# Performance work log

Measured on AMD Instinct MI355X. Metric: run time of the kernel, lower is better.

## Reference

```python
import jax, jax.numpy as jnp
import numpy as np

H = 1024
V = 32000
L = 15
B = 512


def setup_inputs() -> dict:
    key = jax.random.key(0)
    ks = jax.random.split(key, 16)
    s = 0.02
    return {
        "input_ids": jax.random.randint(ks[0], (B,), 0, V),
        "hidden": jax.random.normal(ks[1], (1, B, H), jnp.float32),
        "encoder_outputs": jax.random.normal(ks[2], (L, B, H), jnp.float32),
        "max_length": L,
        "embedding": jax.random.normal(ks[3], (V, H), jnp.float32) * s,
        "attn1_w": jax.random.normal(ks[4], (1, 2 * H), jnp.float32) * s,
        "attn1_b": jnp.zeros((1,), jnp.float32),
        "combine_w": jax.random.normal(ks[5], (H, 2 * H), jnp.float32) * s,
        "combine_b": jnp.zeros((H,), jnp.float32),
        "w_ih": jax.random.normal(ks[6], (3 * H, H), jnp.float32) * s,
        "w_hh": jax.random.normal(ks[7], (3 * H, H), jnp.float32) * s,
        "b_ih": jnp.zeros((3 * H,), jnp.float32),
        "b_hh": jnp.zeros((3 * H,), jnp.float32),
        "out_w": jax.random.normal(ks[8], (V, H), jnp.float32) * s,
        "out_b": jnp.zeros((V,), jnp.float32),
    }


def reference(input_ids, hidden, encoder_outputs, max_length, embedding,
              attn1_w, attn1_b, combine_w, combine_b,
              w_ih, w_hh, b_ih, b_hh, out_w, out_b):
    # embedding lookup (dropout is identity in eval mode)
    emb = embedding[input_ids]                       # [B, H]
    # Bahdanau-style additive scores: vectorize the per-step python loop
    emb_l = jnp.broadcast_to(emb[None], (max_length, B, H))   # [L, B, H]
    cat = jnp.concatenate([emb_l, encoder_outputs], axis=-1)  # [L, B, 2H]
    scores = cat @ attn1_w.T + attn1_b               # [L, B, 1]
    attn_weights = jax.nn.softmax(scores, axis=0)    # softmax over L
    ctx = jnp.sum(attn_weights * encoder_outputs, axis=0)     # [B, H]
    x = jnp.concatenate([emb, ctx], axis=-1) @ combine_w.T + combine_b  # [B, H]
    # n_layers = 1: relu then one GRU step (seq len 1)
    x = jax.nn.relu(x)
    h = hidden[0]                                    # [B, H]
    gi = x @ w_ih.T + b_ih                           # [B, 3H]
    gh = h @ w_hh.T + b_hh                           # [B, 3H]
    i_r, i_z, i_n = jnp.split(gi, 3, axis=1)
    h_r, h_z, h_n = jnp.split(gh, 3, axis=1)
    r = jax.nn.sigmoid(i_r + h_r)
    z = jax.nn.sigmoid(i_z + h_z)
    n = jnp.tanh(i_n + r * h_n)
    h_new = (1.0 - z) * n + z * h                    # [B, H]
    logits = h_new @ out_w.T + out_b                 # [B, V]
    output = jax.nn.log_softmax(logits, axis=1)
    return output, h_new[None], attn_weights
```

## Files before the change

### kernel.cpp

```cpp
#include <hip/hip_runtime.h>

#define HH 1024
#define VV 32000
#define LL 15
#define BB 512

typedef __bf16 bf16;
typedef __bf16 bf16x4 __attribute__((ext_vector_type(4)));
typedef __bf16 bf16x8 __attribute__((ext_vector_type(8)));
typedef float f32x4 __attribute__((ext_vector_type(4)));

#define VMCNT(n) asm volatile("s_waitcnt vmcnt(" #n ")" ::: "memory")
#define SBAR     __builtin_amdgcn_s_barrier()
#define SCHED0   __builtin_amdgcn_sched_barrier(0)

__device__ __forceinline__ unsigned short f2bf(float f) {
    unsigned int u = __float_as_uint(f);
    unsigned int r = (u + 0x7fffu + ((u >> 16) & 1u)) >> 16;
    return (unsigned short)r;
}

__device__ __forceinline__ void gld_lds16(const void* g, void* l) {
    __builtin_amdgcn_global_load_lds(
        (const __attribute__((address_space(1))) unsigned int*)g,
        (__attribute__((address_space(3))) unsigned int*)l, 16, 0, 0);
}

__global__ __launch_bounds__(256)
void pack_w(const float* __restrict__ src, unsigned short* __restrict__ dst) {
    const int bid = blockIdx.x;
    const int g = bid >> 3, rq = bid & 7;
    const float* s0 = src + ((size_t)g * 128 + rq * 16) * 1024;
    unsigned short* d0 = dst + (size_t)g * (16 * 128 * 64);
    #pragma unroll
    for (int j = 0; j < 16; j++) {
        const int s4 = j * 256 + threadIdx.x;
        const f32x4 v = ((const f32x4*)s0)[s4];
        const int sp = s4 * 4;
        const int rl = rq * 16 + (sp >> 10);
        const int k = sp & 1023;
        bf16x4 w = __builtin_convertvector(v, bf16x4);
        *(bf16x4*)&d0[(size_t)(k >> 6) * 8192 + rl * 64 + (k & 63)] = w;
    }
}

__global__ __launch_bounds__(256)
void cvt4_kernel(const float* __restrict__ a0, unsigned short* __restrict__ o0, int n0_,
                 const float* __restrict__ a1, unsigned short* __restrict__ o1, int n1_,
                 const float* __restrict__ a2, unsigned short* __restrict__ o2, int n2_,
                 const float* __restrict__ a3, unsigned short* __restrict__ o3, int n3_) {
    int i = blockIdx.x * 256 + threadIdx.x;
    const float* src; unsigned short* dst;
    if (i < n0_) { src = a0; dst = o0; }
    else if ((i -= n0_) < n1_) { src = a1; dst = o1; }
    else if ((i -= n1_) < n2_) { src = a2; dst = o2; }
    else if ((i -= n2_) < n3_) { src = a3; dst = o3; }
    else return;
    const f32x4 a = ((const f32x4*)src)[2 * i], b = ((const f32x4*)src)[2 * i + 1];
    ((bf16x4*)dst)[2 * i]     = __builtin_convertvector(a, bf16x4);
    ((bf16x4*)dst)[2 * i + 1] = __builtin_convertvector(b, bf16x4);
}

__global__ __launch_bounds__(256)
void attn_kernel(const int* __restrict__ ids, const float* __restrict__ enc,
                 const float* __restrict__ embedding,
                 const float* __restrict__ attn1_w, const float* __restrict__ attn1_b,
                 float* __restrict__ attn_out, unsigned short* __restrict__ cat_out) {
    const int b = blockIdx.x, tid = threadIdx.x;
    const int lane = tid & 63, wv = tid >> 6;

    __shared__ float s_enc[LL * HH];
    __shared__ float s_scores[LL];
    __shared__ float s_red[4];

    for (int idx = tid; idx < LL * HH / 4; idx += 256) {
        const int l = (idx * 4) >> 10, h = (idx * 4) & (HH - 1);
        *(f32x4*)&s_enc[idx * 4] = *(const f32x4*)&enc[((size_t)l * BB + b) * HH + h];
    }

    const float* embr = embedding + (size_t)ids[b] * HH;
    float p = 0.f;
    for (int j = tid; j < HH; j += 256) p += embr[j] * attn1_w[j];
    #pragma unroll
    for (int o = 32; o; o >>= 1) p += __shfl_xor(p, o);
    if (lane == 0) s_red[wv] = p;
    __syncthreads();
    const float semb = s_red[0] + s_red[1] + s_red[2] + s_red[3] + attn1_b[0];

    for (int l = wv; l < LL; l += 4) {
        float q = 0.f;
        for (int j = lane; j < HH; j += 64) q += s_enc[l * HH + j] * attn1_w[HH + j];
        #pragma unroll
        for (int o = 32; o; o >>= 1) q += __shfl_xor(q, o);
        if (lane == 0) s_scores[l] = q + semb;
    }
    __syncthreads();

    float mx = -3.4e38f;
    #pragma unroll
    for (int l = 0; l < LL; l++) mx = fmaxf(mx, s_scores[l]);
    float aw[LL], sum = 0.f;
    #pragma unroll
    for (int l = 0; l < LL; l++) { aw[l] = __expf(s_scores[l] - mx); sum += aw[l]; }
    const float inv = 1.f / sum;
    #pragma unroll
    for (int l = 0; l < LL; l++) aw[l] *= inv;

    if (tid < LL) attn_out[tid * BB + b] = aw[tid];

    for (int j = tid; j < HH; j += 256) {
        float c = 0.f;
        #pragma unroll
        for (int l = 0; l < LL; l++) c += aw[l] * s_enc[l * HH + j];
        cat_out[(size_t)b * (2 * HH) + j] = f2bf(embr[j]);
        cat_out[(size_t)b * (2 * HH) + HH + j] = f2bf(c);
    }
}

template<int TM, int TN, int OUT, int GATES>
__global__ __launch_bounds__(256)
void gemm_nt(const bf16* __restrict__ A, const bf16* __restrict__ B,
             const float* __restrict__ bias, void* __restrict__ Cout,
             const bf16* __restrict__ A2, const bf16* __restrict__ B2,
             const float* __restrict__ bias2, void* __restrict__ C2,
             const int K, const int N) {
    constexpr int FM = TM / 32, FN = TN / 32;
    __shared__ bf16 As[2][TM * 64];
    __shared__ bf16 Bs[2][TN * 64];

    if (GATES && blockIdx.z == 1) { A = A2; B = B2; bias = bias2; Cout = C2; }

    const int tid = threadIdx.x;
    const int lane = tid & 63, wave = tid >> 6;
    const int wm = wave >> 1, wn = wave & 1;
    const int rlo = lane & 15, khi = lane >> 4;
    const int m0 = blockIdx.y * TM, n0 = blockIdx.x * TN;

    f32x4 acc[FM][FN] = {};
    constexpr int IA = TM / 32, IB = TN / 32;

    auto stage = [&](int k0, int buf) {
        #pragma unroll
        for (int i = 0; i < IA; i++) {
            const int p = (i * 256 + tid) * 16;
            const int row = p >> 7;
            const int qs = (p & 127) ^ ((row & 7) << 4);
            gld_lds16(A + (size_t)(m0 + row) * K + k0 + (qs >> 1),
                      &As[buf][0] + i * 2048 + wave * 512);
        }
        #pragma unroll
        for (int i = 0; i < IB; i++) {
            const int p = (i * 256 + tid) * 16;
            const int row = p >> 7;
            const int qs = (p & 127) ^ ((row & 7) << 4);
            gld_lds16(B + (size_t)(n0 + row) * K + k0 + (qs >> 1),
                      &Bs[buf][0] + i * 2048 + wave * 512);
        }
    };

    auto compute = [&](int buf) {
        #pragma unroll
        for (int ks = 0; ks < 2; ks++) {
            bf16x8 af[FM], bfr[FN];
            #pragma unroll
            for (int m = 0; m < FM; m++) {
                const int r = wm * (TM / 2) + m * 16 + rlo;
                const int sw = (ks * 64 + khi * 16) ^ ((r & 7) << 4);
                af[m] = *(const bf16x8*)((const char*)&As[buf][0] + r * 128 + sw);
            }
            #pragma unroll
            for (int n = 0; n < FN; n++) {
                const int r = wn * (TN / 2) + n * 16 + rlo;
                const int sw = (ks * 64 + khi * 16) ^ ((r & 7) << 4);
                bfr[n] = *(const bf16x8*)((const char*)&Bs[buf][0] + r * 128 + sw);
            }
            #pragma unroll
            for (int m = 0; m < FM; m++)
                #pragma unroll
                for (int n = 0; n < FN; n++)
                    acc[m][n] = __builtin_amdgcn_mfma_f32_16x16x32_bf16(af[m], bfr[n], acc[m][n], 0, 0, 0);
        }
    };

    const int NT = K >> 6;
    stage(0, 0);
    stage(64, 1);

    for (int kt = 0; kt < NT; kt += 2) {
        {
            const int t = kt;
            if (t + 1 < NT) { VMCNT(4); } else { VMCNT(0); }
            SCHED0; SBAR; SCHED0;
            compute(0);
            SCHED0; SBAR; SCHED0;
            if (t + 2 < NT) stage((t + 2) << 6, 0);
        }
        {
            const int t = kt + 1;
            if (t + 1 < NT) { VMCNT(4); } else { VMCNT(0); }
            SCHED0; SBAR; SCHED0;
            compute(1);
            SCHED0; SBAR; SCHED0;
            if (t + 2 < NT) stage((t + 2) << 6, 1);
        }
    }

    #pragma unroll
    for (int m = 0; m < FM; m++) {
        const int gr = m0 + wm * (TM / 2) + m * 16 + khi * 4;
        #pragma unroll
        for (int n = 0; n < FN; n++) {
            const int gc = n0 + wn * (TN / 2) + n * 16 + rlo;
            const float bv = bias[gc];
            #pragma unroll
            for (int j = 0; j < 4; j++) {
                float v = acc[m][n][j] + bv;
                if (OUT == 1) {
                    v = fmaxf(v, 0.f);
                    ((unsigned short*)Cout)[(size_t)(gr + j) * N + gc] = f2bf(v);
                } else {
                    ((float*)Cout)[(size_t)(gr + j) * N + gc] = v;
                }
            }
        }
    }
}

__global__ __launch_bounds__(256, 2)
void gemm_out(const bf16* __restrict__ A, const bf16* __restrict__ Bp,
              const float* __restrict__ bias, float* __restrict__ C,
              float* __restrict__ pmax, float* __restrict__ psum) {
    constexpr int K = HH, N = VV;
    __shared__ bf16 As[2][128 * 64];
    __shared__ bf16 Bs[2][128 * 64];
    __shared__ float sPm[2][128], sPs[2][128];

    const int tid = threadIdx.x;
    const int lane = tid & 63, wave = tid >> 6;
    const int wm = wave >> 1, wn = wave & 1;
    const int rlo = lane & 15, khi = lane >> 4;

    constexpr int gridN = 250;
    constexpr int nFull = (gridN >> 3) << 5;
    const int bidx = blockIdx.x;
    int g, jm;
    if (bidx < nFull) { const int s = bidx >> 5, rem = bidx & 31; jm = rem >> 3; g = s * 8 + (rem & 7); }
    else { const int rem = bidx - nFull; constexpr int gleft = gridN & 7; g = (gridN & ~7) + rem % gleft; jm = rem / gleft; }
    const int n0 = g * 128, m0 = jm * 128;

    const char* pb = (const char*)(Bp + (size_t)g * 131072);

    f32x4 acc[4][4] = {};

    auto stage = [&](int k0, int buf) {
        #pragma unroll
        for (int i = 0; i < 4; i++) {
            const int p = (i * 256 + tid) * 16;
            const int row = p >> 7;
            const int qs = (p & 127) ^ ((row & 7) << 4);
            gld_lds16(A + (size_t)(m0 + row) * K + k0 + (qs >> 1),
                      &As[buf][0] + i * 2048 + wave * 512);
        }
        #pragma unroll
        for (int i = 0; i < 4; i++) {
            const int p = (i * 256 + tid) * 16;
            const int row = p >> 7;
            const int qs = (p & 127) ^ ((row & 7) << 4);
            gld_lds16(pb + (size_t)(k0 >> 6) * 16384 + row * 128 + qs,
                      &Bs[buf][0] + i * 2048 + wave * 512);
        }
    };

    auto compute = [&](int buf) {
        #pragma unroll
        for (int ks = 0; ks < 2; ks++) {
            bf16x8 af[4], bfr[4];
            #pragma unroll
            for (int m = 0; m < 4; m++) {
                const int r = wm * 64 + m * 16 + rlo;
                const int sw = (ks * 64 + khi * 16) ^ ((r & 7) << 4);
                af[m] = *(const bf16x8*)((const char*)&As[buf][0] + r * 128 + sw);
            }
            #pragma unroll
            for (int n = 0; n < 4; n++) {
                const int r = wn * 64 + n * 16 + rlo;
                const int sw = (ks * 64 + khi * 16) ^ ((r & 7) << 4);
                bfr[n] = *(const bf16x8*)((const char*)&Bs[buf][0] + r * 128 + sw);
            }
            #pragma unroll
            for (int m = 0; m < 4; m++)
                #pragma unroll
                for (int n = 0; n < 4; n++)
                    acc[m][n] = __builtin_amdgcn_mfma_f32_16x16x32_bf16(af[m], bfr[n], acc[m][n], 0, 0, 0);
        }
    };

    constexpr int NT = K >> 6;
    stage(0, 0);
    stage(64, 1);

    for (int kt = 0; kt < NT; kt += 2) {
        {
            const int t = kt;
            if (t + 1 < NT) { VMCNT(8); } else { VMCNT(0); }
            SCHED0; SBAR; SCHED0;
            compute(0);
            SCHED0; SBAR; SCHED0;
            if (t + 2 < NT) stage((t + 2) << 6, 0);
        }
        {
            const int t = kt + 1;
            if (t + 1 < NT) { VMCNT(8); } else { VMCNT(0); }
            SCHED0; SBAR; SCHED0;
            compute(1);
            SCHED0; SBAR; SCHED0;
            if (t + 2 < NT) stage((t + 2) << 6, 1);
        }
    }

    float bvn[4];
    #pragma unroll
    for (int n = 0; n < 4; n++) bvn[n] = bias[n0 + wn * 64 + n * 16 + rlo];

    #pragma unroll
    for (int m = 0; m < 4; m++) {
        const int rbase = wm * 64 + m * 16 + khi * 4;
        #pragma unroll
        for (int j = 0; j < 4; j++) {
            const int gr = m0 + rbase + j;
            float v[4];
            float lm = -3.4e38f;
            #pragma unroll
            for (int n = 0; n < 4; n++) {
                v[n] = acc[m][n][j] + bvn[n];
                C[(size_t)gr * N + n0 + wn * 64 + n * 16 + rlo] = v[n];
                lm = fmaxf(lm, v[n]);
            }
            #pragma unroll
            for (int o = 8; o; o >>= 1) lm = fmaxf(lm, __shfl_xor(lm, o));
            float ls = 0.f;
            #pragma unroll
            for (int n = 0; n < 4; n++) ls += __expf(v[n] - lm);
            #pragma unroll
            for (int o = 8; o; o >>= 1) ls += __shfl_xor(ls, o);
            if (rlo == 0) { sPm[wn][rbase + j] = lm; sPs[wn][rbase + j] = ls; }
        }
    }
    __syncthreads();
    if (tid < 128) {
        const float ma = sPm[0][tid], mb = sPm[1][tid];
        const float M = fmaxf(ma, mb);
        const float S = sPs[0][tid] * __expf(ma - M) + sPs[1][tid] * __expf(mb - M);
        pmax[(size_t)(m0 + tid) * 256 + g] = M;
        psum[(size_t)(m0 + tid) * 256 + g] = S;
    }
}

__global__ __launch_bounds__(256)
void gru_kernel(const float* __restrict__ gi, const float* __restrict__ gh,
                const float* __restrict__ h, float* __restrict__ hnew,
                unsigned short* __restrict__ hnew_bf) {
    const int i = blockIdx.x * 256 + threadIdx.x;
    const int e = i * 4;
    const int b = e >> 10, j = e & (HH - 1);
    const size_t o = ((size_t)b * 3 * HH + j) / 4;
    const f32x4 ir = ((const f32x4*)gi)[o],          iz = ((const f32x4*)gi)[o + HH / 4],
                in_ = ((const f32x4*)gi)[o + 2 * HH / 4];
    const f32x4 hr = ((const f32x4*)gh)[o],          hz = ((const f32x4*)gh)[o + HH / 4],
                hn = ((const f32x4*)gh)[o + 2 * HH / 4];
    const f32x4 hv = ((const f32x4*)h)[i];
    f32x4 out;
    ushort4 ob;
    #pragma unroll
    for (int c = 0; c < 4; c++) {
        const float r = 1.f / (1.f + __expf(-(ir[c] + hr[c])));
        const float z = 1.f / (1.f + __expf(-(iz[c] + hz[c])));
        const float n = tanhf(in_[c] + r * hn[c]);
        const float v = (1.f - z) * n + z * hv[c];
        out[c] = v;
        ((unsigned short*)&ob)[c] = f2bf(v);
    }
    ((f32x4*)hnew)[i] = out;
    ((ushort4*)hnew_bf)[i] = ob;
}

__global__ __launch_bounds__(512)
void lsm_final(const float* __restrict__ pmax, const float* __restrict__ psum,
               float* __restrict__ logits) {
    const int b = blockIdx.x, tid = threadIdx.x;
    const int lane = tid & 63, wv = tid >> 6;
    __shared__ float sm[8], ss[8];

    float m = -3.4e38f, s = 0.f;
    if (tid < 250) { m = pmax[(size_t)b * 256 + tid]; s = psum[(size_t)b * 256 + tid]; }
    #pragma unroll
    for (int o = 32; o; o >>= 1) {
        const float mo = __shfl_xor(m, o), so = __shfl_xor(s, o);
        const float nm = fmaxf(m, mo);
        s = s * __expf(m - nm) + so * __expf(mo - nm);
        m = nm;
    }
    if (lane == 0) { sm[wv] = m; ss[wv] = s; }
    __syncthreads();
    float M = sm[0], S;
    #pragma unroll
    for (int w = 1; w < 8; w++) M = fmaxf(M, sm[w]);
    S = ss[0] * __expf(sm[0] - M);
    #pragma unroll
    for (int w = 1; w < 8; w++) S += ss[w] * __expf(sm[w] - M);
    const float lse = M + __logf(S);

    float* row = logits + (size_t)b * VV;
    for (int j = tid; j < VV / 4; j += 512) {
        f32x4 v = ((const f32x4*)row)[j];
        v[0] -= lse; v[1] -= lse; v[2] -= lse; v[3] -= lse;
        ((f32x4*)row)[j] = v;
    }
}

extern "C" void kernel_launch(void* const* d_in, const int* in_sizes, int n_in,
                              void* d_out, int out_size, void* d_ws, size_t ws_size,
                              hipStream_t stream) {
    const int*   ids       = (const int*)d_in[0];
    const float* hidden    = (const float*)d_in[1];
    const float* enc       = (const float*)d_in[2];
    const float* embedding = (const float*)d_in[4];
    const float* attn1_w   = (const float*)d_in[5];
    const float* attn1_b   = (const float*)d_in[6];
    const float* combine_w = (const float*)d_in[7];
    const float* combine_b = (const float*)d_in[8];
    const float* w_ih      = (const float*)d_in[9];
    const float* w_hh      = (const float*)d_in[10];
    const float* b_ih      = (const float*)d_in[11];
    const float* b_hh      = (const float*)d_in[12];
    const float* out_w     = (const float*)d_in[13];
    const float* out_b     = (const float*)d_in[14];

    float* out_lsm = (float*)d_out;
    float* out_h   = out_lsm + (size_t)BB * VV;
    float* out_aw  = out_h + (size_t)BB * HH;

    char* w = (char*)d_ws;
    unsigned short* packed   = (unsigned short*)w;   w += (size_t)VV * HH * 2;
    unsigned short* w_ih_bf  = (unsigned short*)w;   w += (size_t)3 * HH * HH * 2;
    unsigned short* w_hh_bf  = (unsigned short*)w;   w += (size_t)3 * HH * HH * 2;
    unsigned short* w_cb_bf  = (unsigned short*)w;   w += (size_t)2 * HH * HH * 2;
    unsigned short* cat_bf   = (unsigned short*)w;   w += (size_t)BB * 2 * HH * 2;
    unsigned short* x_bf     = (unsigned short*)w;   w += (size_t)BB * HH * 2;
    unsigned short* hid_bf   = (unsigned short*)w;   w += (size_t)BB * HH * 2;
    unsigned short* hnew_bf  = (unsigned short*)w;   w += (size_t)BB * HH * 2;
    float* gi   = (float*)w;                         w += (size_t)BB * 3 * HH * 4;
    float* gh   = (float*)w;                         w += (size_t)BB * 3 * HH * 4;
    float* pmax = (float*)w;                         w += (size_t)BB * 256 * 4;
    float* psum = (float*)w;                         w += (size_t)BB * 256 * 4;

    pack_w<<<2000, 256, 0, stream>>>(out_w, packed);
    cvt4_kernel<<<(3 * HH * HH / 8 * 2 + 2 * HH * HH / 8 + BB * HH / 8) / 256, 256, 0, stream>>>(
        w_ih, w_ih_bf, 3 * HH * HH / 8,
        w_hh, w_hh_bf, 3 * HH * HH / 8,
        combine_w, w_cb_bf, 2 * HH * HH / 8,
        hidden, hid_bf, BB * HH / 8);

    attn_kernel<<<BB, 256, 0, stream>>>(ids, enc, embedding, attn1_w, attn1_b, out_aw, cat_bf);

    gemm_nt<64, 64, 1, 0><<<dim3(HH / 64, BB / 64), 256, 0, stream>>>(
        (const bf16*)cat_bf, (const bf16*)w_cb_bf, combine_b, x_bf,
        nullptr, nullptr, nullptr, nullptr, 2 * HH, HH);

    gemm_nt<64, 64, 0, 1><<<dim3(3 * HH / 64, BB / 64, 2), 256, 0, stream>>>(
        (const bf16*)hid_bf, (const bf16*)w_hh_bf, b_hh, gh,
        (const bf16*)x_bf, (const bf16*)w_ih_bf, b_ih, gi, HH, 3 * HH);

    gru_kernel<<<(BB * HH / 4) / 256, 256, 0, stream>>>(gi, gh, hidden, out_h, hnew_bf);

    gemm_out<<<1000, 256, 0, stream>>>(
        (const bf16*)hnew_bf, (const bf16*)packed, out_b, out_lsm, pmax, psum);

    lsm_final<<<BB, 512, 0, stream>>>(pmax, psum, out_lsm);
}
```

Measured before the change: 182.2 us.

## Fuse prologue kernels and merge output GEMM with log-softmax via grid barrier

Merges the weight-packing, fp32-to-bf16 conversion and attention kernels into one prologue launch. The output GEMM now uses 256x256 tiles with 512 threads and 250 blocks, pre-swizzles the packed weight layout, and finishes with an atomic-counter grid barrier. After the barrier each block combines the per-tile max/sum partials and writes the final log-softmax directly. This removes the logits write-then-reread pass and two launches, but the spin barrier assumes all 250 blocks are co-resident, and the larger tiles may hurt occupancy.

```diff
diff --git a/kernel.cpp b/kernel.cpp
--- a/kernel.cpp
+++ b/kernel.cpp
@@ -26,52 +26,59 @@
         (__attribute__((address_space(3))) unsigned int*)l, 16, 0, 0);
 }
 
+#define NPACKB 2000
+#define NCVTB  4352
+
 __global__ __launch_bounds__(256)
-void pack_w(const float* __restrict__ src, unsigned short* __restrict__ dst) {
-    const int bid = blockIdx.x;
-    const int g = bid >> 3, rq = bid & 7;
-    const float* s0 = src + ((size_t)g * 128 + rq * 16) * 1024;
-    unsigned short* d0 = dst + (size_t)g * (16 * 128 * 64);
-    #pragma unroll
-    for (int j = 0; j < 16; j++) {
-        const int s4 = j * 256 + threadIdx.x;
-        const f32x4 v = ((const f32x4*)s0)[s4];
-        const int sp = s4 * 4;
-        const int rl = rq * 16 + (sp >> 10);
-        const int k = sp & 1023;
-        bf16x4 w = __builtin_convertvector(v, bf16x4);
-        *(bf16x4*)&d0[(size_t)(k >> 6) * 8192 + rl * 64 + (k & 63)] = w;
-    }
-}
-
-__global__ __launch_bounds__(256)
-void cvt4_kernel(const float* __restrict__ a0, unsigned short* __restrict__ o0, int n0_,
-                 const float* __restrict__ a1, unsigned short* __restrict__ o1, int n1_,
-                 const float* __restrict__ a2, unsigned short* __restrict__ o2, int n2_,
-                 const float* __restrict__ a3, unsigned short* __restrict__ o3, int n3_) {
-    int i = blockIdx.x * 256 + threadIdx.x;
-    const float* src; unsigned short* dst;
-    if (i < n0_) { src = a0; dst = o0; }
-    else if ((i -= n0_) < n1_) { src = a1; dst = o1; }
-    else if ((i -= n1_) < n2_) { src = a2; dst = o2; }
-    else if ((i -= n2_) < n3_) { src = a3; dst = o3; }
-    else return;
-    const f32x4 a = ((const f32x4*)src)[2 * i], b = ((const f32x4*)src)[2 * i + 1];
-    ((bf16x4*)dst)[2 * i]     = __builtin_convertvector(a, bf16x4);
-    ((bf16x4*)dst)[2 * i + 1] = __builtin_convertvector(b, bf16x4);
-}
-
-__global__ __launch_bounds__(256)
-void attn_kernel(const int* __restrict__ ids, const float* __restrict__ enc,
-                 const float* __restrict__ embedding,
-                 const float* __restrict__ attn1_w, const float* __restrict__ attn1_b,
-                 float* __restrict__ attn_out, unsigned short* __restrict__ cat_out) {
-    const int b = blockIdx.x, tid = threadIdx.x;
-    const int lane = tid & 63, wv = tid >> 6;
-
+void prologue(const float* __restrict__ out_w, unsigned short* __restrict__ packed,
+              const float* __restrict__ w_ih, unsigned short* __restrict__ w_ih_bf,
+              const float* __restrict__ w_hh, unsigned short* __restrict__ w_hh_bf,
+              const float* __restrict__ combine_w, unsigned short* __restrict__ w_cb_bf,
+              const float* __restrict__ hidden, unsigned short* __restrict__ hid_bf,
+              const int* __restrict__ ids, const float* __restrict__ enc,
+              const float* __restrict__ embedding,
+              const float* __restrict__ attn1_w, const float* __restrict__ attn1_b,
+              float* __restrict__ attn_out, unsigned short* __restrict__ cat_out) {
     __shared__ float s_enc[LL * HH];
     __shared__ float s_scores[LL];
     __shared__ float s_red[4];
+
+    const int bid = blockIdx.x, tid = threadIdx.x;
+
+    if (bid < NPACKB) {
+        const int g = bid >> 4, rq = bid & 15;
+        const float* s0 = out_w + ((size_t)g * 256 + rq * 16) * 1024;
+        char* pd = (char*)packed + (size_t)g * 524288;
+        #pragma unroll
+        for (int j = 0; j < 16; j++) {
+            const int s4 = j * 256 + tid;
+            const f32x4 v = ((const f32x4*)s0)[s4];
+            const int sp = s4 * 4;
+            const int r = rq * 16 + (sp >> 10);
+            const int k = sp & 1023;
+            bf16x4 w = __builtin_convertvector(v, bf16x4);
+            *(bf16x4*)(pd + (size_t)(k >> 6) * 32768 + r * 128 + (((k & 63) * 2) ^ ((r & 7) << 4))) = w;
+        }
+        return;
+    }
+    if (bid < NPACKB + NCVTB) {
+        int i = (bid - NPACKB) * 256 + tid;
+        const float* src; unsigned short* dst;
+        const int n0_ = 3 * HH * HH / 8, n1_ = 3 * HH * HH / 8;
+        const int n2_ = 2 * HH * HH / 8, n3_ = BB * HH / 8;
+        if (i < n0_) { src = w_ih; dst = w_ih_bf; }
+        else if ((i -= n0_) < n1_) { src = w_hh; dst = w_hh_bf; }
+        else if ((i -= n1_) < n2_) { src = combine_w; dst = w_cb_bf; }
+        else if ((i -= n2_) < n3_) { src = hidden; dst = hid_bf; }
+        else return;
+        const f32x4 a = ((const f32x4*)src)[2 * i], b = ((const f32x4*)src)[2 * i + 1];
+        ((bf16x4*)dst)[2 * i]     = __builtin_convertvector(a, bf16x4);
+        ((bf16x4*)dst)[2 * i + 1] = __builtin_convertvector(b, bf16x4);
+        return;
+    }
+
+    const int b = bid - (NPACKB + NCVTB);
+    const int lane = tid & 63, wv = tid >> 6;
 
     for (int idx = tid; idx < LL * HH / 4; idx += 256) {
         const int l = (idx * 4) >> 10, h = (idx * 4) & (HH - 1);
@@ -226,141 +233,12 @@
     }
 }
 
-__global__ __launch_bounds__(256, 2)
-void gemm_out(const bf16* __restrict__ A, const bf16* __restrict__ Bp,
-              const float* __restrict__ bias, float* __restrict__ C,
-              float* __restrict__ pmax, float* __restrict__ psum) {
-    constexpr int K = HH, N = VV;
-    __shared__ bf16 As[2][128 * 64];
-    __shared__ bf16 Bs[2][128 * 64];
-    __shared__ float sPm[2][128], sPs[2][128];
-
-    const int tid = threadIdx.x;
-    const int lane = tid & 63, wave = tid >> 6;
-    const int wm = wave >> 1, wn = wave & 1;
-    const int rlo = lane & 15, khi = lane >> 4;
-
-    constexpr int gridN = 250;
-    constexpr int nFull = (gridN >> 3) << 5;
-    const int bidx = blockIdx.x;
-    int g, jm;
-    if (bidx < nFull) { const int s = bidx >> 5, rem = bidx & 31; jm = rem >> 3; g = s * 8 + (rem & 7); }
-    else { const int rem = bidx - nFull; constexpr int gleft = gridN & 7; g = (gridN & ~7) + rem % gleft; jm = rem / gleft; }
-    const int n0 = g * 128, m0 = jm * 128;
-
-    const char* pb = (const char*)(Bp + (size_t)g * 131072);
-
-    f32x4 acc[4][4] = {};
-
-    auto stage = [&](int k0, int buf) {
-        #pragma unroll
-        for (int i = 0; i < 4; i++) {
-            const int p = (i * 256 + tid) * 16;
-            const int row = p >> 7;
-            const int qs = (p & 127) ^ ((row & 7) << 4);
-            gld_lds16(A + (size_t)(m0 + row) * K + k0 + (qs >> 1),
-                      &As[buf][0] + i * 2048 + wave * 512);
-        }
-        #pragma unroll
-        for (int i = 0; i < 4; i++) {
-            const int p = (i * 256 + tid) * 16;
-            const int row = p >> 7;
-            const int qs = (p & 127) ^ ((row & 7) << 4);
-            gld_lds16(pb + (size_t)(k0 >> 6) * 16384 + row * 128 + qs,
-                      &Bs[buf][0] + i * 2048 + wave * 512);
-        }
-    };
-
-    auto compute = [&](int buf) {
-        #pragma unroll
-        for (int ks = 0; ks < 2; ks++) {
-            bf16x8 af[4], bfr[4];
-            #pragma unroll
-            for (int m = 0; m < 4; m++) {
-                const int r = wm * 64 + m * 16 + rlo;
-                const int sw = (ks * 64 + khi * 16) ^ ((r & 7) << 4);
-                af[m] = *(const bf16x8*)((const char*)&As[buf][0] + r * 128 + sw);
-            }
-            #pragma unroll
-            for (int n = 0; n < 4; n++) {
-                const int r = wn * 64 + n * 16 + rlo;
-                const int sw = (ks * 64 + khi * 16) ^ ((r & 7) << 4);
-                bfr[n] = *(const bf16x8*)((const char*)&Bs[buf][0] + r * 128 + sw);
-            }
-            #pragma unroll
-            for (int m = 0; m < 4; m++)
-                #pragma unroll
-                for (int n = 0; n < 4; n++)
-                    acc[m][n] = __builtin_amdgcn_mfma_f32_16x16x32_bf16(af[m], bfr[n], acc[m][n], 0, 0, 0);
-        }
-    };
-
-    constexpr int NT = K >> 6;
-    stage(0, 0);
-    stage(64, 1);
-
-    for (int kt = 0; kt < NT; kt += 2) {
-        {
-            const int t = kt;
-            if (t + 1 < NT) { VMCNT(8); } else { VMCNT(0); }
-            SCHED0; SBAR; SCHED0;
-            compute(0);
-            SCHED0; SBAR; SCHED0;
-            if (t + 2 < NT) stage((t + 2) << 6, 0);
-        }
-        {
-            const int t = kt + 1;
-            if (t + 1 < NT) { VMCNT(8); } else { VMCNT(0); }
-            SCHED0; SBAR; SCHED0;
-            compute(1);
-            SCHED0; SBAR; SCHED0;
-            if (t + 2 < NT) stage((t + 2) << 6, 1);
-        }
-    }
-
-    float bvn[4];
-    #pragma unroll
-    for (int n = 0; n < 4; n++) bvn[n] = bias[n0 + wn * 64 + n * 16 + rlo];
-
-    #pragma unroll
-    for (int m = 0; m < 4; m++) {
-        const int rbase = wm * 64 + m * 16 + khi * 4;
-        #pragma unroll
-        for (int j = 0; j < 4; j++) {
-            const int gr = m0 + rbase + j;
-            float v[4];
-            float lm = -3.4e38f;
-            #pragma unroll
-            for (int n = 0; n < 4; n++) {
-                v[n] = acc[m][n][j] + bvn[n];
-                C[(size_t)gr * N + n0 + wn * 64 + n * 16 + rlo] = v[n];
-                lm = fmaxf(lm, v[n]);
-            }
-            #pragma unroll
-            for (int o = 8; o; o >>= 1) lm = fmaxf(lm, __shfl_xor(lm, o));
-            float ls = 0.f;
-            #pragma unroll
-            for (int n = 0; n < 4; n++) ls += __expf(v[n] - lm);
-            #pragma unroll
-            for (int o = 8; o; o >>= 1) ls += __shfl_xor(ls, o);
-            if (rlo == 0) { sPm[wn][rbase + j] = lm; sPs[wn][rbase + j] = ls; }
-        }
-    }
-    __syncthreads();
-    if (tid < 128) {
-        const float ma = sPm[0][tid], mb = sPm[1][tid];
-        const float M = fmaxf(ma, mb);
-        const float S = sPs[0][tid] * __expf(ma - M) + sPs[1][tid] * __expf(mb - M);
-        pmax[(size_t)(m0 + tid) * 256 + g] = M;
-        psum[(size_t)(m0 + tid) * 256 + g] = S;
-    }
-}
-
 __global__ __launch_bounds__(256)
 void gru_kernel(const float* __restrict__ gi, const float* __restrict__ gh,
                 const float* __restrict__ h, float* __restrict__ hnew,
-                unsigned short* __restrict__ hnew_bf) {
+                unsigned short* __restrict__ hnew_bf, int* __restrict__ ctr) {
     const int i = blockIdx.x * 256 + threadIdx.x;
+    if (i == 0) *ctr = 0;
     const int e = i * 4;
     const int b = e >> 10, j = e & (HH - 1);
     const size_t o = ((size_t)b * 3 * HH + j) / 4;
@@ -385,36 +263,162 @@
 }
 
 __global__ __launch_bounds__(512)
-void lsm_final(const float* __restrict__ pmax, const float* __restrict__ psum,
-               float* __restrict__ logits) {
-    const int b = blockIdx.x, tid = threadIdx.x;
-    const int lane = tid & 63, wv = tid >> 6;
-    __shared__ float sm[8], ss[8];
-
-    float m = -3.4e38f, s = 0.f;
-    if (tid < 250) { m = pmax[(size_t)b * 256 + tid]; s = psum[(size_t)b * 256 + tid]; }
-    #pragma unroll
-    for (int o = 32; o; o >>= 1) {
-        const float mo = __shfl_xor(m, o), so = __shfl_xor(s, o);
-        const float nm = fmaxf(m, mo);
-        s = s * __expf(m - nm) + so * __expf(mo - nm);
-        m = nm;
-    }
-    if (lane == 0) { sm[wv] = m; ss[wv] = s; }
-    __syncthreads();
-    float M = sm[0], S;
-    #pragma unroll
-    for (int w = 1; w < 8; w++) M = fmaxf(M, sm[w]);
-    S = ss[0] * __expf(sm[0] - M);
-    #pragma unroll
-    for (int w = 1; w < 8; w++) S += ss[w] * __expf(sm[w] - M);
-    const float lse = M + __logf(S);
-
-    float* row = logits + (size_t)b * VV;
-    for (int j = tid; j < VV / 4; j += 512) {
-        f32x4 v = ((const f32x4*)row)[j];
-        v[0] -= lse; v[1] -= lse; v[2] -= lse; v[3] -= lse;
-        ((f32x4*)row)[j] = v;
+void gemm_lsm(const bf16* __restrict__ A, const bf16* __restrict__ Bp,
+              const float* __restrict__ bias, float* __restrict__ C,
+              float* __restrict__ pmax, float* __restrict__ psum,
+              int* __restrict__ ctr) {
+    constexpr int K = HH, N = VV;
+    __shared__ bf16 As[2][256 * 64];
+    __shared__ bf16 Bs[2][256 * 64];
+    __shared__ float sPm[2][256], sPs[2][256], sLse[256];
+
+    const int tid = threadIdx.x;
+    const int lane = tid & 63, wave = tid >> 6;
+    const int wm = wave >> 1, wn = wave & 1;
+    const int rlo = lane & 15, khi = lane >> 4;
+
+    constexpr int gridN = 125;
+    constexpr int nFull = (gridN >> 3) << 4;
+    const int bidx = blockIdx.x;
+    int g, jm;
+    if (bidx < nFull) { const int s = bidx >> 4, rem = bidx & 15; jm = rem >> 3; g = s * 8 + (rem & 7); }
+    else { const int rem = bidx - nFull; constexpr int gleft = gridN & 7; g = (gridN & ~7) + rem % gleft; jm = rem / gleft; }
+    const int n0 = g * 256, m0 = jm * 256;
+
+    const char* pb = (const char*)Bp + (size_t)g * 524288;
+
+    f32x4 acc[4][8] = {};
+
+    auto stage = [&](int k0, int buf) {
+        #pragma unroll
+        for (int i = 0; i < 4; i++) {
+            const int p = (i * 8 + wave) * 1024 + lane * 16;
+            const int row = p >> 7;
+            const int qs = (p & 127) ^ ((row & 7) << 4);
+            gld_lds16(A + (size_t)(m0 + row) * K + k0 + (qs >> 1),
+                      (char*)&As[buf][0] + (i * 8 + wave) * 1024);
+        }
+        #pragma unroll
+        for (int i = 0; i < 4; i++) {
+            const int off = (i * 8 + wave) * 1024;
+            gld_lds16(pb + (size_t)(k0 >> 6) * 32768 + off + lane * 16,
+                      (char*)&Bs[buf][0] + off);
+        }
+    };
+
+    auto compute = [&](int buf) {
+        #pragma unroll
+        for (int ks = 0; ks < 2; ks++) {
+            bf16x8 af[4], bfr[8];
+            #pragma unroll
+            for (int m = 0; m < 4; m++) {
+                const int r = wm * 64 + m * 16 + rlo;
+                const int sw = (ks * 64 + khi * 16) ^ ((r & 7) << 4);
+                af[m] = *(const bf16x8*)((const char*)&As[buf][0] + r * 128 + sw);
+            }
+            #pragma unroll
+            for (int n = 0; n < 8; n++) {
+                const int r = wn * 128 + n * 16 + rlo;
+                const int sw = (ks * 64 + khi * 16) ^ ((r & 7) << 4);
+                bfr[n] = *(const bf16x8*)((const char*)&Bs[buf][0] + r * 128 + sw);
+            }
+            #pragma unroll
+            for (int m = 0; m < 4; m++)
+                #pragma unroll
+                for (int n = 0; n < 8; n++)
+                    acc[m][n] = __builtin_amdgcn_mfma_f32_16x16x32_bf16(af[m], bfr[n], acc[m][n], 0, 0, 0);
+        }
+    };
+
+    constexpr int NT = K >> 6;
+    stage(0, 0);
+    stage(64, 1);
+
+    for (int kt = 0; kt < NT; kt += 2) {
+        {
+            const int t = kt;
+            if (t + 1 < NT) { VMCNT(8); } else { VMCNT(0); }
+            SCHED0; SBAR; SCHED0;
+            compute(0);
+            SCHED0; SBAR; SCHED0;
+            if (t + 2 < NT) stage((t + 2) << 6, 0);
+        }
+        {
+            const int t = kt + 1;
+            if (t + 1 < NT) { VMCNT(8); } else { VMCNT(0); }
+            SCHED0; SBAR; SCHED0;
+            compute(1);
+            SCHED0; SBAR; SCHED0;
+            if (t + 2 < NT) stage((t + 2) << 6, 1);
+        }
+    }
+
+    float bvn[8];
+    #pragma unroll
+    for (int n = 0; n < 8; n++) bvn[n] = bias[n0 + wn * 128 + n * 16 + rlo];
+
+    #pragma unroll
+    for (int m = 0; m < 4; m++) {
+        #pragma unroll
+        for (int j = 0; j < 4; j++) {
+            const int lr = wm * 64 + m * 16 + khi * 4 + j;
+            float lm = -3.4e38f;
+            float v[8];
+            #pragma unroll
+            for (int n = 0; n < 8; n++) { v[n] = acc[m][n][j] + bvn[n]; lm = fmaxf(lm, v[n]); }
+            #pragma unroll
+            for (int o = 8; o; o >>= 1) lm = fmaxf(lm, __shfl_xor(lm, o));
+            float ls = 0.f;
+            #pragma unroll
+            for (int n = 0; n < 8; n++) ls += __expf(v[n] - lm);
+            #pragma unroll
+            for (int o = 8; o; o >>= 1) ls += __shfl_xor(ls, o);
+            if (rlo == 0) { sPm[wn][lr] = lm; sPs[wn][lr] = ls; }
+        }
+    }
+    __syncthreads();
+    if (tid < 256) {
+        const float ma = sPm[0][tid], mb = sPm[1][tid];
+        const float M = fmaxf(ma, mb);
+        const float S = sPs[0][tid] * __expf(ma - M) + sPs[1][tid] * __expf(mb - M);
+        pmax[(size_t)(m0 + tid) * 128 + g] = M;
+        psum[(size_t)(m0 + tid) * 128 + g] = S;
+    }
+    __threadfence();
+    __syncthreads();
+
+    if (tid == 0) {
+        atomicAdd(ctr, 1);
+        while (atomicAdd(ctr, 0) < 250) __builtin_amdgcn_s_sleep(32);
+    }
+    __syncthreads();
+    __threadfence();
+
+    if (tid < 256) {
+        const int gr = m0 + tid;
+        float m = -3.4e38f, s = 0.f;
+        for (int g2 = 0; g2 < 125; g2++) {
+            const float mo = pmax[(size_t)gr * 128 + g2];
+            const float so = psum[(size_t)gr * 128 + g2];
+            const float nm = fmaxf(m, mo);
+            s = s * __expf(m - nm) + so * __expf(mo - nm);
+            m = nm;
+        }
+        sLse[tid] = m + __logf(s);
+    }
+    __syncthreads();
+
+    #pragma unroll
+    for (int m = 0; m < 4; m++) {
+        #pragma unroll
+        for (int j = 0; j < 4; j++) {
+            const int lr = wm * 64 + m * 16 + khi * 4 + j;
+            const float lse = sLse[lr];
+            const size_t rbase = (size_t)(m0 + lr) * N + n0 + wn * 128;
+            #pragma unroll
+            for (int n = 0; n < 8; n++)
+                C[rbase + n * 16 + rlo] = acc[m][n][j] + bvn[n] - lse;
+        }
     }
 }
 
@@ -451,17 +455,13 @@
     unsigned short* hnew_bf  = (unsigned short*)w;   w += (size_t)BB * HH * 2;
     float* gi   = (float*)w;                         w += (size_t)BB * 3 * HH * 4;
     float* gh   = (float*)w;                         w += (size_t)BB * 3 * HH * 4;
-    float* pmax = (float*)w;                         w += (size_t)BB * 256 * 4;
-    float* psum = (float*)w;                         w += (size_t)BB * 256 * 4;
-
-    pack_w<<<2000, 256, 0, stream>>>(out_w, packed);
-    cvt4_kernel<<<(3 * HH * HH / 8 * 2 + 2 * HH * HH / 8 + BB * HH / 8) / 256, 256, 0, stream>>>(
-        w_ih, w_ih_bf, 3 * HH * HH / 8,
-        w_hh, w_hh_bf, 3 * HH * HH / 8,
-        combine_w, w_cb_bf, 2 * HH * HH / 8,
-        hidden, hid_bf, BB * HH / 8);
-
-    attn_kernel<<<BB, 256, 0, stream>>>(ids, enc, embedding, attn1_w, attn1_b, out_aw, cat_bf);
+    float* pmax = (float*)w;                         w += (size_t)BB * 128 * 4;
+    float* psum = (float*)w;                         w += (size_t)BB * 128 * 4;
+    int*   ctr  = (int*)w;                           w += 256;
+
+    prologue<<<NPACKB + NCVTB + BB, 256, 0, stream>>>(
+        out_w, packed, w_ih, w_ih_bf, w_hh, w_hh_bf, combine_w, w_cb_bf,
+        hidden, hid_bf, ids, enc, embedding, attn1_w, attn1_b, out_aw, cat_bf);
 
     gemm_nt<64, 64, 1, 0><<<dim3(HH / 64, BB / 64), 256, 0, stream>>>(
         (const bf16*)cat_bf, (const bf16*)w_cb_bf, combine_b, x_bf,
@@ -471,10 +471,8 @@
         (const bf16*)hid_bf, (const bf16*)w_hh_bf, b_hh, gh,
         (const bf16*)x_bf, (const bf16*)w_ih_bf, b_ih, gi, HH, 3 * HH);
 
-    gru_kernel<<<(BB * HH / 4) / 256, 256, 0, stream>>>(gi, gh, hidden, out_h, hnew_bf);
-
-    gemm_out<<<1000, 256, 0, stream>>>(
-        (const bf16*)hnew_bf, (const bf16*)packed, out_b, out_lsm, pmax, psum);
-
-    lsm_final<<<BB, 512, 0, stream>>>(pmax, psum, out_lsm);
-}
+    gru_kernel<<<(BB * HH / 4) / 256, 256, 0, stream>>>(gi, gh, hidden, out_h, hnew_bf, ctr);
+
+    gemm_lsm<<<250, 512, 0, stream>>>(
+        (const bf16*)hnew_bf, (const bf16*)packed, out_b, out_lsm, pmax, psum, ctr);
+}
```

Result: slower. 250.2 us (+37.3%).

## Merge prologue kernels and stage logits in bf16 before log-softmax

Applied to the files above, without the earlier changes.

Folds the weight packing, bf16 conversion and attention kernels into one launch, branching on block index, to cut launch gaps. When the workspace is large enough, the output GEMM writes logits as bf16 to a scratch buffer. The final log-softmax pass then reads that buffer and writes fp32 to the output, so the 65MB fp32 logits are written once and read back at half width. The cost is bf16 rounding of the logits, which is a precision loss in the output, and a larger workspace requirement.

```diff
diff --git a/kernel.cpp b/kernel.cpp
--- a/kernel.cpp
+++ b/kernel.cpp
@@ -19,6 +19,9 @@
     unsigned int r = (u + 0x7fffu + ((u >> 16) & 1u)) >> 16;
     return (unsigned short)r;
 }
+__device__ __forceinline__ float bf2f(unsigned short u) {
+    return __uint_as_float(((unsigned int)u) << 16);
+}
 
 __device__ __forceinline__ void gld_lds16(const void* g, void* l) {
     __builtin_amdgcn_global_load_lds(
@@ -26,52 +29,59 @@
         (__attribute__((address_space(3))) unsigned int*)l, 16, 0, 0);
 }
 
+#define NPACKB 2000
+#define NCVTB  4352
+
 __global__ __launch_bounds__(256)
-void pack_w(const float* __restrict__ src, unsigned short* __restrict__ dst) {
-    const int bid = blockIdx.x;
-    const int g = bid >> 3, rq = bid & 7;
-    const float* s0 = src + ((size_t)g * 128 + rq * 16) * 1024;
-    unsigned short* d0 = dst + (size_t)g * (16 * 128 * 64);
-    #pragma unroll
-    for (int j = 0; j < 16; j++) {
-        const int s4 = j * 256 + threadIdx.x;
-        const f32x4 v = ((const f32x4*)s0)[s4];
-        const int sp = s4 * 4;
-        const int rl = rq * 16 + (sp >> 10);
-        const int k = sp & 1023;
-        bf16x4 w = __builtin_convertvector(v, bf16x4);
-        *(bf16x4*)&d0[(size_t)(k >> 6) * 8192 + rl * 64 + (k & 63)] = w;
-    }
-}
-
-__global__ __launch_bounds__(256)
-void cvt4_kernel(const float* __restrict__ a0, unsigned short* __restrict__ o0, int n0_,
-                 const float* __restrict__ a1, unsigned short* __restrict__ o1, int n1_,
-                 const float* __restrict__ a2, unsigned short* __restrict__ o2, int n2_,
-                 const float* __restrict__ a3, unsigned short* __restrict__ o3, int n3_) {
-    int i = blockIdx.x * 256 + threadIdx.x;
-    const float* src; unsigned short* dst;
-    if (i < n0_) { src = a0; dst = o0; }
-    else if ((i -= n0_) < n1_) { src = a1; dst = o1; }
-    else if ((i -= n1_) < n2_) { src = a2; dst = o2; }
-    else if ((i -= n2_) < n3_) { src = a3; dst = o3; }
-    else return;
-    const f32x4 a = ((const f32x4*)src)[2 * i], b = ((const f32x4*)src)[2 * i + 1];
-    ((bf16x4*)dst)[2 * i]     = __builtin_convertvector(a, bf16x4);
-    ((bf16x4*)dst)[2 * i + 1] = __builtin_convertvector(b, bf16x4);
-}
-
-__global__ __launch_bounds__(256)
-void attn_kernel(const int* __restrict__ ids, const float* __restrict__ enc,
-                 const float* __restrict__ embedding,
-                 const float* __restrict__ attn1_w, const float* __restrict__ attn1_b,
-                 float* __restrict__ attn_out, unsigned short* __restrict__ cat_out) {
-    const int b = blockIdx.x, tid = threadIdx.x;
-    const int lane = tid & 63, wv = tid >> 6;
-
+void prologue(const float* __restrict__ out_w, unsigned short* __restrict__ packed,
+              const float* __restrict__ w_ih, unsigned short* __restrict__ w_ih_bf,
+              const float* __restrict__ w_hh, unsigned short* __restrict__ w_hh_bf,
+              const float* __restrict__ combine_w, unsigned short* __restrict__ w_cb_bf,
+              const float* __restrict__ hidden, unsigned short* __restrict__ hid_bf,
+              const int* __restrict__ ids, const float* __restrict__ enc,
+              const float* __restrict__ embedding,
+              const float* __restrict__ attn1_w, const float* __restrict__ attn1_b,
+              float* __restrict__ attn_out, unsigned short* __restrict__ cat_out) {
     __shared__ float s_enc[LL * HH];
     __shared__ float s_scores[LL];
     __shared__ float s_red[4];
+
+    const int bid = blockIdx.x, tid = threadIdx.x;
+
+    if (bid < NPACKB) {
+        const int g = bid >> 3, rq = bid & 7;
+        const float* s0 = out_w + ((size_t)g * 128 + rq * 16) * 1024;
+        unsigned short* d0 = packed + (size_t)g * (16 * 128 * 64);
+        #pragma unroll
+        for (int j = 0; j < 16; j++) {
+            const int s4 = j * 256 + tid;
+            const f32x4 v = ((const f32x4*)s0)[s4];
+            const int sp = s4 * 4;
+            const int rl = rq * 16 + (sp >> 10);
+            const int k = sp & 1023;
+            bf16x4 w = __builtin_convertvector(v, bf16x4);
+            *(bf16x4*)&d0[(size_t)(k >> 6) * 8192 + rl * 64 + (k & 63)] = w;
+        }
+        return;
+    }
+    if (bid < NPACKB + NCVTB) {
+        int i = (bid - NPACKB) * 256 + tid;
+        const float* src; unsigned short* dst;
+        const int n0_ = 3 * HH * HH / 8, n1_ = 3 * HH * HH / 8;
+        const int n2_ = 2 * HH * HH / 8, n3_ = BB * HH / 8;
+        if (i < n0_) { src = w_ih; dst = w_ih_bf; }
+        else if ((i -= n0_) < n1_) { src = w_hh; dst = w_hh_bf; }
+        else if ((i -= n1_) < n2_) { src = combine_w; dst = w_cb_bf; }
+        else if ((i -= n2_) < n3_) { src = hidden; dst = hid_bf; }
+        else return;
+        const f32x4 a = ((const f32x4*)src)[2 * i], b = ((const f32x4*)src)[2 * i + 1];
+        ((bf16x4*)dst)[2 * i]     = __builtin_convertvector(a, bf16x4);
+        ((bf16x4*)dst)[2 * i + 1] = __builtin_convertvector(b, bf16x4);
+        return;
+    }
+
+    const int b = bid - (NPACKB + NCVTB);
+    const int lane = tid & 63, wv = tid >> 6;
 
     for (int idx = tid; idx < LL * HH / 4; idx += 256) {
         const int l = (idx * 4) >> 10, h = (idx * 4) & (HH - 1);
@@ -226,9 +236,11 @@
     }
 }
 
+template<int CB>
 __global__ __launch_bounds__(256, 2)
 void gemm_out(const bf16* __restrict__ A, const bf16* __restrict__ Bp,
               const float* __restrict__ bias, float* __restrict__ C,
+              unsigned short* __restrict__ Cb,
               float* __restrict__ pmax, float* __restrict__ psum) {
     constexpr int K = HH, N = VV;
     __shared__ bf16 As[2][128 * 64];
@@ -333,7 +345,8 @@
             #pragma unroll
             for (int n = 0; n < 4; n++) {
                 v[n] = acc[m][n][j] + bvn[n];
-                C[(size_t)gr * N + n0 + wn * 64 + n * 16 + rlo] = v[n];
+                const size_t ci = (size_t)gr * N + n0 + wn * 64 + n * 16 + rlo;
+                if (CB) Cb[ci] = f2bf(v[n]); else C[ci] = v[n];
                 lm = fmaxf(lm, v[n]);
             }
             #pragma unroll
@@ -384,9 +397,10 @@
     ((ushort4*)hnew_bf)[i] = ob;
 }
 
+template<int CB>
 __global__ __launch_bounds__(512)
 void lsm_final(const float* __restrict__ pmax, const float* __restrict__ psum,
-               float* __restrict__ logits) {
+               const unsigned short* __restrict__ Cb, float* __restrict__ logits) {
     const int b = blockIdx.x, tid = threadIdx.x;
     const int lane = tid & 63, wv = tid >> 6;
     __shared__ float sm[8], ss[8];
@@ -411,10 +425,25 @@
     const float lse = M + __logf(S);
 
     float* row = logits + (size_t)b * VV;
-    for (int j = tid; j < VV / 4; j += 512) {
-        f32x4 v = ((const f32x4*)row)[j];
-        v[0] -= lse; v[1] -= lse; v[2] -= lse; v[3] -= lse;
-        ((f32x4*)row)[j] = v;
+    if (CB) {
+        const unsigned short* rowc = Cb + (size_t)b * VV;
+        for (int j = tid; j < VV / 8; j += 512) {
+            const ushort4 u0 = ((const ushort4*)rowc)[2 * j];
+            const ushort4 u1 = ((const ushort4*)rowc)[2 * j + 1];
+            f32x4 v0, v1;
+            v0[0] = bf2f(u0.x) - lse; v0[1] = bf2f(u0.y) - lse;
+            v0[2] = bf2f(u0.z) - lse; v0[3] = bf2f(u0.w) - lse;
+            v1[0] = bf2f(u1.x) - lse; v1[1] = bf2f(u1.y) - lse;
+            v1[2] = bf2f(u1.z) - lse; v1[3] = bf2f(u1.w) - lse;
+            ((f32x4*)row)[2 * j] = v0;
+            ((f32x4*)row)[2 * j + 1] = v1;
+        }
+    } else {
+        for (int j = tid; j < VV / 4; j += 512) {
+            f32x4 v = ((const f32x4*)row)[j];
+            v[0] -= lse; v[1] -= lse; v[2] -= lse; v[3] -= lse;
+            ((f32x4*)row)[j] = v;
+        }
     }
 }
 
@@ -453,15 +482,13 @@
     float* gh   = (float*)w;                         w += (size_t)BB * 3 * HH * 4;
     float* pmax = (float*)w;                         w += (size_t)BB * 256 * 4;
     float* psum = (float*)w;                         w += (size_t)BB * 256 * 4;
-
-    pack_w<<<2000, 256, 0, stream>>>(out_w, packed);
-    cvt4_kernel<<<(3 * HH * HH / 8 * 2 + 2 * HH * HH / 8 + BB * HH / 8) / 256, 256, 0, stream>>>(
-        w_ih, w_ih_bf, 3 * HH * HH / 8,
-        w_hh, w_hh_bf, 3 * HH * HH / 8,
-        combine_w, w_cb_bf, 2 * HH * HH / 8,
-        hidden, hid_bf, BB * HH / 8);
-
-    attn_kernel<<<BB, 256, 0, stream>>>(ids, enc, embedding, attn1_w, attn1_b, out_aw, cat_bf);
+    unsigned short* Cb = (unsigned short*)w;
+    const size_t needed_cb = (size_t)(w - (char*)d_ws) + (size_t)BB * VV * 2;
+    const bool use_cb = ws_size >= needed_cb;
+
+    prologue<<<NPACKB + NCVTB + BB, 256, 0, stream>>>(
+        out_w, packed, w_ih, w_ih_bf, w_hh, w_hh_bf, combine_w, w_cb_bf,
+        hidden, hid_bf, ids, enc, embedding, attn1_w, attn1_b, out_aw, cat_bf);
 
     gemm_nt<64, 64, 1, 0><<<dim3(HH / 64, BB / 64), 256, 0, stream>>>(
         (const bf16*)cat_bf, (const bf16*)w_cb_bf, combine_b, x_bf,
@@ -473,8 +500,13 @@
 
     gru_kernel<<<(BB * HH / 4) / 256, 256, 0, stream>>>(gi, gh, hidden, out_h, hnew_bf);
 
-    gemm_out<<<1000, 256, 0, stream>>>(
-        (const bf16*)hnew_bf, (const bf16*)packed, out_b, out_lsm, pmax, psum);
-
-    lsm_final<<<BB, 512, 0, stream>>>(pmax, psum, out_lsm);
-}
+    if (use_cb) {
+        gemm_out<1><<<1000, 256, 0, stream>>>(
+            (const bf16*)hnew_bf, (const bf16*)packed, out_b, nullptr, Cb, pmax, psum);
+        lsm_final<1><<<BB, 512, 0, stream>>>(pmax, psum, Cb, out_lsm);
+    } else {
+        gemm_out<0><<<1000, 256, 0, stream>>>(
+            (const bf16*)hnew_bf, (const bf16*)packed, out_b, out_lsm, nullptr, pmax, psum);
+        lsm_final<0><<<BB, 512, 0, stream>>>(pmax, psum, nullptr, out_lsm);
+    }
+}
```

Result: faster. 171.9 us (median of 2 runs) (-5.7%).
